# Kernel optimization log

Hardware: AMD Instinct MI355X
Metric: run time of the kernel (lower is better)

## Reference

```python
import jax, jax.numpy as jnp
import numpy as np

GAMMA = 0.9          # EMA momentum for prototype update
N_CLASSES = 201      # 200 classes + 1 background
K_PROTO = 5          # prototypes per class
FG_THRESH = 0.5      # pca_fg_threshold
SK_EPS = 0.05        # sinkhorn temperature (SwAV-style)
SK_ITERS = 3         # sinkhorn iterations
PCA_ITERS = 10       # niter of torch.pca_lowrank


def _l2norm(x, axis=-1):
    return x / jnp.maximum(jnp.linalg.norm(x, axis=axis, keepdims=True), 1e-12)


def _pca_first_component(X, key):
    # Randomized power iteration for the top left singular vector of the
    # centered data (mirrors torch.pca_lowrank(X, q=1, center=True, niter=10)).
    Xc = X - X.mean(0, keepdims=True)            # [N, D]
    G = Xc.T @ Xc                                # [D, D]
    v = jax.random.normal(key, (X.shape[1],), X.dtype)
    v = v / jnp.linalg.norm(v)
    def body(v, _):
        v = G @ v
        return v / jnp.maximum(jnp.linalg.norm(v), 1e-12), None
    v, _ = jax.lax.scan(body, v, None, length=PCA_ITERS)
    u = Xc @ v                                   # [N]
    return u / jnp.maximum(jnp.linalg.norm(u), 1e-12)


def _masked_sinkhorn(logits, mask):
    # logits: [C, BN, K], mask: [C, BN] bool (rows belonging to class c).
    # Vectorized equivalent of the per-class sinkhorn_knopp(L_c): returns a
    # row-stochastic assignment on the masked rows, balanced over the K cols.
    tiny = 1e-9
    m = mask[..., None].astype(logits.dtype)     # [C, BN, 1]
    Q = jnp.exp(logits / SK_EPS) * m
    n_c = jnp.maximum(mask.sum(-1).astype(logits.dtype), 1.0)[:, None, None]
    K = Q.shape[-1]
    Q = Q / jnp.maximum(Q.sum((-2, -1), keepdims=True), tiny)
    for _ in range(SK_ITERS):
        Q = Q / jnp.maximum(Q.sum(-2, keepdims=True), tiny) / K   # balance cols
        Q = Q * m
        Q = Q / jnp.maximum(Q.sum(-1, keepdims=True), tiny) / n_c # balance rows
        Q = Q * m
    return Q * n_c  # each masked row sums to 1


def setup_inputs() -> dict:
    key = jax.random.key(0)
    k1, k2, k3 = jax.random.split(key, 3)
    B, n_patches, dim = 32, 1024, 768
    patch_tokens = jax.random.normal(k1, (B, n_patches, dim), jnp.float32)
    prototypes = 0.02 * jax.random.normal(k2, (N_CLASSES, K_PROTO, dim), jnp.float32)
    labels = jax.random.randint(k3, (B,), 0, 200).astype(jnp.int64)
    return {"patch_tokens": patch_tokens, "prototypes": prototypes, "labels": labels}


def reference(patch_tokens, prototypes, labels):
    B, n_patches, D = patch_tokens.shape

    pt_norm = _l2norm(patch_tokens)              # [B, N, D]
    proto_norm = _l2norm(prototypes)             # [C, K, D]
    # B n_patches dim, C K dim -> B n_patches C K
    logits = jnp.einsum('bnd,ckd->bnck', pt_norm, proto_norm)

    # ---- get_pseudo_patch_labels (PCA foreground extraction) ----
    X = patch_tokens.reshape(-1, D)
    U = _pca_first_component(X, jax.random.key(1))
    U_scaled = (U - U.min()) / (U.max() - U.min())
    fg = (U_scaled < FG_THRESH).reshape(B, n_patches)
    patch_labels = jnp.where(fg, labels[:, None], N_CLASSES - 1)  # [B, N] int

    # ---- update_prototypes, vectorized over the 201-class python loop ----
    pl_flat = patch_labels.reshape(-1)                            # [B*N]
    L = jnp.transpose(logits.reshape(-1, N_CLASSES, K_PROTO), (1, 0, 2))  # [C, BN, K]
    class_ids = jnp.arange(N_CLASSES)
    mask = pl_flat[None, :] == class_ids[:, None]                 # [C, BN]
    Q = _masked_sinkhorn(L, mask)                                 # [C, BN, K]
    # P_c_new = L_c_assignment.T @ I_c, batched over classes
    P_new = jnp.einsum('cnk,nd->ckd', Q, pt_norm.reshape(-1, D))  # [C, K, D]
    present = (labels[None, :] == class_ids[:, None]).any(-1)     # 'c in labels'
    ema = GAMMA * prototypes + (1.0 - GAMMA) * P_new              # momentum_update
    new_prototypes = jnp.where(present[:, None, None], ema, prototypes)

    image_prototype_logits = logits.max(1)        # [B, C, K]
    class_logits = image_prototype_logits.sum(-1) # [B, C]
    return class_logits, image_prototype_logits, new_prototypes
```

## Files before the change

kernel.cpp:

```cpp
#include <hip/hip_runtime.h>
#include <stdint.h>
#include <stddef.h>

#define DEV static __device__ __forceinline__

typedef __attribute__((ext_vector_type(8))) short bf16x8;
typedef __attribute__((ext_vector_type(4))) float f32x4;
typedef __attribute__((ext_vector_type(4))) int i32x4;

DEV float bf2f(unsigned short u){ union{unsigned int i; float f;} v; v.i = ((unsigned int)u)<<16; return v.f; }
DEV unsigned short f2bf(float f){ union{float f; unsigned int i;} v; v.f=f; unsigned int i=v.i;
  return (unsigned short)((i + 0x7FFFu + ((i>>16)&1u)) >> 16); }
DEV unsigned int fenc(float x){ unsigned int i = __float_as_uint(x); return (i & 0x80000000u) ? ~i : (i | 0x80000000u); }
DEV float fdec(unsigned int e){ unsigned int i = (e & 0x80000000u) ? (e & 0x7FFFFFFFu) : ~e; return __uint_as_float(i); }

DEV float waveSum(float s){
  for (int m=32;m;m>>=1) s += __shfl_xor(s, m, 64);
  return s;
}

DEV float blockSum(float v, float* red){
  int t = threadIdx.x;
  red[t] = v; __syncthreads();
  for (int k=128;k>0;k>>=1){ if (t<k) red[t] += red[t+k]; __syncthreads(); }
  float r = red[0]; __syncthreads();
  return r;
}

DEV void gl16(const void* g, void* lds){
  __builtin_amdgcn_global_load_lds(
      (const __attribute__((address_space(1))) void*)g,
      (__attribute__((address_space(3))) void*)lds, 16, 0, 0);
}

DEV float erfinv_f(float x){
  float w = -log1pf(-__fmul_rn(x,x));
  float p;
  if (w < 5.0f){
    w = w - 2.5f;
    p = 2.81022636e-08f;
    p = 3.43273939e-07f + p*w;
    p = -3.5233877e-06f + p*w;
    p = -4.39150654e-06f + p*w;
    p = 0.00021858087f + p*w;
    p = -0.00125372503f + p*w;
    p = -0.00417768164f + p*w;
    p = 0.246640727f + p*w;
    p = 1.50140941f + p*w;
  } else {
    w = sqrtf(w) - 3.0f;
    p = -0.000200214257f;
    p = 0.000100950558f + p*w;
    p = 0.00134934322f + p*w;
    p = -0.00367342844f + p*w;
    p = 0.00573950773f + p*w;
    p = -0.0076224613f + p*w;
    p = 0.00943887047f + p*w;
    p = 1.00167406f + p*w;
    p = 2.83297682f + p*w;
  }
  return p*x;
}

#define BN_TOT 32768
#define DIM 768
#define NCLS 201
#define KP 5
#define CKPAD 1024
#define NSPLIT_G 16
#define GSPLIT 32
#define PSPLIT 8
#define NBLK_G 672


__global__ void k_setup(unsigned int* ipl_enc, int* cnt, int* cur, int* present,
                        unsigned int* minmax, float* meansum,
                        const int* __restrict__ raw, int* __restrict__ lab,
                        float* __restrict__ v,
                        const float* __restrict__ protos, unsigned short* __restrict__ protn,
                        int* __restrict__ dcnt){
  int i = blockIdx.x*256 + threadIdx.x;
  ipl_enc[i] = 0u;
  if (i < NCLS){ cnt[i]=0; cur[i]=0; present[i]=0; }
  if (i < DIM) meansum[i] = 0.f;
  if (i == 0){
    minmax[0]=0xFFFFFFFFu; minmax[1]=0u;
    dcnt[0] = 0;
    bool is64 = true;
    for (int j=0;j<8;j++){
      int lo = raw[2*j], hi = raw[2*j+1];
      if (hi != 0 || lo < 0 || lo >= NCLS-1){ is64 = false; break; }
    }
    for (int j=0;j<32;j++) lab[j] = is64 ? raw[2*j] : raw[j];
  }
  if (i < DIM){
    unsigned int ks[3] = {0u, 1u, 0x1BD11BDBu};
    const int rot0[4] = {13,15,26,6};
    const int rot1[4] = {17,29,16,24};
    unsigned int x0 = 0u, x1 = (unsigned int)i;
    x0 += ks[0]; x1 += ks[1];
    #pragma unroll
    for (int g=0; g<5; g++){
      const int* rr = (g&1) ? rot1 : rot0;
      #pragma unroll
      for (int j=0;j<4;j++){
        x0 += x1;
        x1 = (x1 << rr[j]) | (x1 >> (32-rr[j]));
        x1 ^= x0;
      }
      x0 += ks[(g+1)%3];
      x1 += ks[(g+2)%3] + (unsigned int)(g+1);
    }
    unsigned int b = x0 ^ x1;
    const float lo = __uint_as_float(0xBF7FFFFFu);
    const float sq2 = __uint_as_float(0x3FB504F3u);
    float f = __uint_as_float((b>>9) | 0x3F800000u) - 1.0f;
    float uu = __fadd_rn(__fmul_rn(f, 2.0f), lo);
    uu = fmaxf(lo, uu);
    v[i] = sq2 * erfinv_f(uu);
  }
  int l = threadIdx.x & 63;
  #pragma unroll
  for (int rr=0; rr<2; rr++){
    int row = blockIdx.x*8 + (threadIdx.x>>6)*2 + rr;
    if (row >= NCLS*KP){
      for (int j=0;j<12;j++) protn[(size_t)row*DIM + l + j*64] = 0;
    } else {
      const float* p = protos + (size_t)row*DIM;
      float x[12]; float s = 0.f;
      for (int j=0;j<12;j++){ x[j] = p[l + j*64]; s += x[j]*x[j]; }
      s = waveSum(s);
      float inv = 1.0f / fmaxf(sqrtf(s), 1e-12f);
      for (int j=0;j<12;j++) protn[(size_t)row*DIM + l + j*64] = f2bf(x[j]*inv);
    }
  }
}

__global__ void k_trans(const float* __restrict__ X, signed char* __restrict__ q1T,
                        signed char* __restrict__ q2T, float* __restrict__ meansum){
  __shared__ float tile[64][65];
  __shared__ float colsum[4][64];
  int n0 = blockIdx.x*64, c0 = blockIdx.y*64;
  int t = threadIdx.x;
  float part = 0.f;
  for (int i=0;i<16;i++){
    int idx = t + i*256; int r = idx>>6, c = idx&63;
    float x = X[(size_t)(n0+r)*DIM + c0+c];
    tile[r][c] = x;
    part += x;
  }
  colsum[t>>6][t&63] = part;
  __syncthreads();
  for (int i=0;i<4;i++){
    int flat = t + i*256;
    int c = flat>>4;
    int ng = flat&15;
    unsigned int p1 = 0, p2 = 0;
    #pragma unroll
    for (int j=0;j<4;j++){
      float x = tile[ng*4+j][c];
      int q1 = (int)rintf(x*16.0f);
      q1 = max(-127, min(127, q1));
      float r2 = x - (float)q1*(1.0f/16.0f);
      int q2 = (int)rintf(r2*2048.0f);
      q2 = max(-127, min(127, q2));
      p1 |= ((unsigned int)(q1 & 0xff)) << (8*j);
      p2 |= ((unsigned int)(q2 & 0xff)) << (8*j);
    }
    size_t o = (size_t)(c0+c)*BN_TOT + n0 + ng*4;
    *(unsigned int*)&q1T[o] = p1;
    *(unsigned int*)&q2T[o] = p2;
  }
  if (t < 64){
    float s = colsum[0][t]+colsum[1][t]+colsum[2][t]+colsum[3][t];
    atomicAdd(&meansum[c0+t], s);
  }
}

__global__ void k_ptn(const float* __restrict__ X, unsigned short* __restrict__ ptn){
  int row = blockIdx.x*4 + (threadIdx.x>>6);
  int l = threadIdx.x & 63;
  const float4* xr = (const float4*)(X + (size_t)row*DIM);
  float4 x4[3]; float s = 0.f;
  #pragma unroll
  for (int j=0;j<3;j++){
    x4[j] = xr[l + j*64];
    s += x4[j].x*x4[j].x + x4[j].y*x4[j].y + x4[j].z*x4[j].z + x4[j].w*x4[j].w;
  }
  s = waveSum(s);
  float inv = 1.0f / fmaxf(sqrtf(s), 1e-12f);
  #pragma unroll
  for (int j=0;j<3;j++){
    ushort4 o;
    o.x = f2bf(x4[j].x*inv); o.y = f2bf(x4[j].y*inv);
    o.z = f2bf(x4[j].z*inv); o.w = f2bf(x4[j].w*inv);
    *(ushort4*)&ptn[(size_t)row*DIM + 4*(l + j*64)] = o;
  }
}

DEV void g_coords(int b, int& s, int& ib, int& jb){
  int xcd = b & 7, q = b >> 3;
  s = xcd + 8*(q/21);
  int p = q % 21;
  ib = 0; int rem = p;
  while (rem >= 6 - ib){ rem -= 6 - ib; ib++; }
  jb = ib + rem;
}

__global__ __launch_bounds__(256) void k_mega(const signed char* __restrict__ q1T,
                                              const signed char* __restrict__ q2T,
                                              float* __restrict__ Gpart,
                                              const unsigned short* __restrict__ A,
                                              const unsigned short* __restrict__ Bt,
                                              unsigned int* __restrict__ ipl_enc){
  __shared__ __align__(16) signed char LB[32768];
  __shared__ float red[2][2][64];
  int bid = blockIdx.x;
  int t = threadIdx.x, w = t>>6, l = t&63;
  int wr = w>>1, wc = w&1;

  if (bid < NBLK_G){
    int chain2 = (bid >= 21*NSPLIT_G);
    int s, ib, jb; g_coords(chain2 ? bid - 21*NSPLIT_G : bid, s, ib, jb);
    size_t baseA = (size_t)(ib*128)*BN_TOT;
    size_t baseB = (size_t)(jb*128)*BN_TOT;

    i32x4 acc[4][4];
    #pragma unroll
    for (int m=0;m<4;m++)
      #pragma unroll
      for (int n=0;n<4;n++){ acc[m][n][0]=0; acc[m][n][1]=0; acc[m][n][2]=0; acc[m][n][3]=0; }

    float scale;
    if (!chain2){
      signed char* A1 = LB;
      signed char* B1 = LB + 16384;
      int gu = (l&7) ^ ((l>>3)&7);
      size_t lane_off = (size_t)(l>>3)*BN_TOT + (size_t)gu*16;
      for (int kt=0; kt<16; kt++){
        size_t k0 = (size_t)s*2048 + (size_t)kt*128;
        __syncthreads();
        #pragma unroll
        for (int ci=0; ci<4; ci++){
          int rg = w + ci*4;
          size_t roff = (size_t)(rg*8)*BN_TOT + k0 + lane_off;
          gl16(q1T + baseA + roff, A1 + rg*1024);
          gl16(q1T + baseB + roff, B1 + rg*1024);
        }
        __syncthreads();
        #pragma unroll
        for (int kk=0; kk<2; kk++){
          int physb = (((kk*4) + (l>>4)) ^ (l&7))*16;
          i32x4 b1[4];
          #pragma unroll
          for (int n=0;n<4;n++) b1[n] = *(const i32x4*)&B1[(wc*64 + n*16 + (l&15))*128 + physb];
          #pragma unroll
          for (int m=0;m<4;m++){
            i32x4 a1 = *(const i32x4*)&A1[(wr*64 + m*16 + (l&15))*128 + physb];
            #pragma unroll
            for (int n=0;n<4;n++)
              acc[m][n] = __builtin_amdgcn_mfma_i32_16x16x64_i8(a1, b1[n], acc[m][n], 0,0,0);
          }
        }
      }
      scale = 1.0f/256.0f;
    } else {
      signed char* A1 = LB;
      signed char* A2 = LB + 8192;
      signed char* B1 = LB + 16384;
      signed char* B2 = LB + 24576;
      int gu = (l&3) ^ ((l>>2)&3) ^ (l>>4);
      size_t lane_off = (size_t)(l>>2)*BN_TOT + (size_t)gu*16;
      int physc = (l>>4) ^ (l&3) ^ ((l>>2)&3);
      int rdA = (wr*64 + (l&15))*64 + physc*16;
      int rdB = (wc*64 + (l&15))*64 + physc*16;
      for (int kt=0; kt<32; kt++){
        size_t k0 = (size_t)s*2048 + (size_t)kt*64;
        __syncthreads();
        #pragma unroll
        for (int ci=0; ci<2; ci++){
          int c = w + ci*4;
          size_t roff = (size_t)(c*16)*BN_TOT + k0 + lane_off;
          gl16(q1T + baseA + roff, A1 + c*1024);
          gl16(q2T + baseA + roff, A2 + c*1024);
          gl16(q1T + baseB + roff, B1 + c*1024);
          gl16(q2T + baseB + roff, B2 + c*1024);
        }
        __syncthreads();
        i32x4 b1[4], b2[4];
        #pragma unroll
        for (int n=0;n<4;n++){
          b1[n] = *(const i32x4*)&B1[rdB + n*1024];
          b2[n] = *(const i32x4*)&B2[rdB + n*1024];
        }
        #pragma unroll
        for (int m=0;m<4;m++){
          i32x4 a1 = *(const i32x4*)&A1[rdA + m*1024];
          i32x4 a2 = *(const i32x4*)&A2[rdA + m*1024];
          #pragma unroll
          for (int n=0;n<4;n++){
            acc[m][n] = __builtin_amdgcn_mfma_i32_16x16x64_i8(a1, b2[n], acc[m][n], 0,0,0);
            acc[m][n] = __builtin_amdgcn_mfma_i32_16x16x64_i8(a2, b1[n], acc[m][n], 0,0,0);
          }
        }
      }
      scale = 1.0f/32768.0f;
    }

    int slice = chain2 ? (NSPLIT_G + s) : s;
    float* out = Gpart + (size_t)slice*DIM*DIM;
    #pragma unroll
    for (int m=0;m<4;m++)
      #pragma unroll
      for (int n=0;n<4;n++)
        #pragma unroll
        for (int r=0;r<4;r++){
          int row = ib*128 + wr*64 + m*16 + (l>>4)*4 + r;
          int col = jb*128 + wc*64 + n*16 + (l&15);
          float val = (float)acc[m][n][r]*scale;
          out[(size_t)row*DIM + col] = val;
          if (ib != jb) out[(size_t)col*DIM + row] = val;
        }
  } else {
    unsigned short* As = (unsigned short*)LB;
    unsigned short* Bs = (unsigned short*)(LB + 16384);
    int flat = bid - NBLK_G;
    int xcd = flat & 7, j = flat >> 3;
    int mb = xcd*32 + (j>>3);
    int nb = j & 7;

    int gu = (l&7) ^ ((l>>3)&7);
    size_t lane_off = (size_t)(l>>3)*DIM + (size_t)gu*8;
    size_t baseA = (size_t)(mb*128)*DIM;
    size_t baseB = (size_t)(nb*128)*DIM;

    f32x4 acc[4][4];
    #pragma unroll
    for (int m=0;m<4;m++)
      #pragma unroll
      for (int n=0;n<4;n++){ acc[m][n][0]=0.f; acc[m][n][1]=0.f; acc[m][n][2]=0.f; acc[m][n][3]=0.f; }

    for (int kt=0; kt<12; kt++){
      size_t k0 = (size_t)kt*64;
      __syncthreads();
      #pragma unroll
      for (int ci=0; ci<4; ci++){
        int rg = w + ci*4;
        size_t roff = (size_t)(rg*8)*DIM + k0 + lane_off;
        gl16(A + baseA + roff, &As[rg*512]);
        gl16(Bt + baseB + roff, &Bs[rg*512]);
      }
      __syncthreads();
      #pragma unroll
      for (int kk=0; kk<2; kk++){
        int physb = (((kk*4) + (l>>4)) ^ (l&7))*8;
        bf16x8 a[4], b[4];
        #pragma unroll
        for (int m=0;m<4;m++) a[m] = *(const bf16x8*)&As[(wr*64 + m*16 + (l&15))*64 + physb];
        #pragma unroll
        for (int n=0;n<4;n++) b[n] = *(const bf16x8*)&Bs[(wc*64 + n*16 + (l&15))*64 + physb];
        #pragma unroll
        for (int m=0;m<4;m++)
          #pragma unroll
          for (int n=0;n<4;n++)
            acc[m][n] = __builtin_amdgcn_mfma_f32_16x16x32_bf16(a[m], b[n], acc[m][n], 0,0,0);
      }
    }
    float vmax[4];
    #pragma unroll
    for (int n=0;n<4;n++){
      float v = -1e30f;
      #pragma unroll
      for (int m=0;m<4;m++)
        #pragma unroll
        for (int r=0;r<4;r++) v = fmaxf(v, acc[m][n][r]);
      v = fmaxf(v, __shfl_xor(v, 16, 64));
      v = fmaxf(v, __shfl_xor(v, 32, 64));
      vmax[n] = v;
    }
    __syncthreads();
    if (l < 16){
      #pragma unroll
      for (int n=0;n<4;n++) red[wc][wr][n*16 + l] = vmax[n];
    }
    __syncthreads();
    if (t < 128){
      int wcc = t>>6, col = t&63;
      float v = fmaxf(red[wcc][0][col], red[wcc][1][col]);
      int gcol = nb*128 + wcc*64 + col;
      if (gcol < NCLS*KP){
        int b = (mb*128) >> 10;
        atomicMax(&ipl_enc[b*CKPAD + gcol], fenc(v));
      }
    }
  }
}

__global__ void k_gfix(const float* __restrict__ Gpart, const float* __restrict__ meansum,
                       float* __restrict__ G){
  int i4 = blockIdx.x*256 + threadIdx.x;
  int i = i4*4;
  int r = i/DIM, c = i%DIM;
  float4 s = make_float4(0.f,0.f,0.f,0.f);
  for (int p=0;p<GSPLIT;p++){
    float4 g = *(const float4*)&Gpart[(size_t)p*DIM*DIM + i];
    s.x += g.x; s.y += g.y; s.z += g.z; s.w += g.w;
  }
  const float invN = 1.0f/32768.0f;
  float mr = meansum[r]*invN;
  float4 mc = *(const float4*)&meansum[c];
  float4 o;
  o.x = s.x*invN - mr*mc.x*invN;
  o.y = s.y*invN - mr*mc.y*invN;
  o.z = s.z*invN - mr*mc.z*invN;
  o.w = s.w*invN - mr*mc.w*invN;
  *(float4*)&G[i] = o;
}

__global__ void k_mv(const float* __restrict__ G, const float* __restrict__ vin,
                     float* __restrict__ vout){
  __shared__ float vs[DIM];
  int t = threadIdx.x;
  for (int i=t;i<DIM;i+=256) vs[i] = vin[i];
  __syncthreads();
  int row = blockIdx.x*4 + (t>>6), l = t&63;
  const float* g = G + (size_t)row*DIM;
  float s = 0.f;
  for (int j=0;j<12;j++) s += g[l + j*64]*vs[l + j*64];
  s = waveSum(s);
  if (l==0) vout[row] = s;
}

__global__ void k_u(const float* __restrict__ X, const float* __restrict__ v,
                    const float* __restrict__ meansum,
                    float* __restrict__ u, unsigned int* __restrict__ minmax){
  __shared__ float vs[DIM];
  __shared__ float red[256];
  __shared__ float smn[4], smx[4];
  int t = threadIdx.x;
  for (int i=t;i<DIM;i+=256) vs[i] = v[i];
  __syncthreads();
  float ps = 0.f;
  for (int i=t;i<DIM;i+=256) ps += meansum[i]*(1.0f/32768.0f)*vs[i];
  float scal = blockSum(ps, red);
  int w = t>>6, l = t&63;
  float mn = 1e30f, mx = -1e30f;
  #pragma unroll
  for (int rr=0; rr<4; rr++){
    int row = blockIdx.x*16 + w*4 + rr;
    const float4* xr = (const float4*)(X + (size_t)row*DIM);
    float s = 0.f;
    #pragma unroll
    for (int j=0;j<3;j++){
      float4 x4 = xr[l + j*64];
      int base = 4*(l + j*64);
      s += x4.x*vs[base] + x4.y*vs[base+1] + x4.z*vs[base+2] + x4.w*vs[base+3];
    }
    s = waveSum(s);
    if (l==0){
      float val = s - scal;
      u[row] = val;
      mn = fminf(mn, val); mx = fmaxf(mx, val);
    }
  }
  if (l==0){ smn[w]=mn; smx[w]=mx; }
  __syncthreads();
  if (t==0){
    for (int k=1;k<4;k++){ mn = fminf(mn, smn[k]); mx = fmaxf(mx, smx[k]); }
    atomicMin(&minmax[0], fenc(mn));
    atomicMax(&minmax[1], fenc(mx));
  }
}

__global__ void k_pl(const float* __restrict__ u, const int* __restrict__ labels,
                     const unsigned int* __restrict__ minmax, int* __restrict__ pl,
                     int* __restrict__ cnt, int* __restrict__ offs,
                     int* __restrict__ present, int* __restrict__ dcnt){
  int n = blockIdx.x*256 + threadIdx.x;
  int t = threadIdx.x;
  float umin = fdec(minmax[0]), umax = fdec(minmax[1]);
  float us = (u[n]-umin)/(umax-umin);
  int c = (us < 0.5f) ? labels[n>>10] : (NCLS-1);
  pl[n] = c;
  if (c < NCLS-1) atomicAdd(&cnt[c], 1);
  __threadfence();
  __shared__ int lastblk;
  if (t == 0) lastblk = (atomicAdd(dcnt, 1) == 127) ? 1 : 0;
  __syncthreads();
  if (lastblk){
    __shared__ int sc[256];
    sc[t] = (t < NCLS-1) ? atomicAdd(&cnt[t], 0) : 0;
    __syncthreads();
    for (int d=1; d<256; d<<=1){
      int v = (t >= d) ? sc[t-d] : 0;
      __syncthreads();
      sc[t] += v;
      __syncthreads();
    }
    if (t < NCLS) offs[t] = (t == 0) ? 0 : sc[t-1];
    if (t < 32) atomicOr(&present[labels[t]], 1);
  }
}

__global__ void k_scatter(const int* __restrict__ pl, const int* __restrict__ offs,
                          int* __restrict__ cur, int* __restrict__ idx){
  int n = blockIdx.x*256 + threadIdx.x;
  int c = pl[n];
  if (c < NCLS-1){
    int p = offs[c] + atomicAdd(&cur[c], 1);
    idx[p] = n;
  }
}

__global__ void k_qlog(const int* __restrict__ idx, const int* __restrict__ offs,
                       const int* __restrict__ pl, const unsigned short* __restrict__ ptn,
                       const unsigned short* __restrict__ protn, float* __restrict__ q){
  int i = blockIdx.x*4 + (threadIdx.x>>6);
  int l = threadIdx.x & 63;
  int total = offs[NCLS-1];
  if (i >= total) return;
  int n = idx[i];
  int c = pl[n];
  const unsigned short* pr = ptn + (size_t)n*DIM;
  float x[12];
  for (int j=0;j<12;j++) x[j] = bf2f(pr[l + j*64]);
  for (int k=0;k<KP;k++){
    const unsigned short* wv = protn + (size_t)(c*KP + k)*DIM;
    float s = 0.f;
    for (int j=0;j<12;j++) s += x[j]*bf2f(wv[l + j*64]);
    s = waveSum(s);
    if (l==0) q[(size_t)i*KP + k] = expf(s*20.0f);
  }
}

__global__ void k_sink(const int* __restrict__ cnt, const int* __restrict__ offs,
                       float* __restrict__ q){
  __shared__ float red[256];
  __shared__ float colf[KP];
  int c = blockIdx.x;
  int nc = cnt[c];
  if (nc == 0) return;
  int n0 = offs[c];
  float* Q = q + (size_t)n0*KP;
  int t = threadIdx.x;
  int tot5 = nc*KP;
  float s = 0.f;
  for (int i=t;i<tot5;i+=256) s += Q[i];
  float total = blockSum(s, red);
  float sc = 1.0f/fmaxf(total, 1e-9f);
  for (int i=t;i<tot5;i+=256) Q[i] *= sc;
  __syncthreads();
  float ncf = (float)nc;
  for (int it=0; it<3; it++){
    float cs[KP] = {0,0,0,0,0};
    for (int i=t;i<nc;i+=256){
      const float* row = Q + (size_t)i*KP;
      #pragma unroll
      for (int k=0;k<KP;k++) cs[k] += row[k];
    }
    for (int k=0;k<KP;k++){
      float v = blockSum(cs[k], red);
      if (t==0) colf[k] = 1.0f/(fmaxf(v,1e-9f)*(float)KP);
    }
    __syncthreads();
    for (int i=t;i<nc;i+=256){
      float* row = Q + (size_t)i*KP;
      float qq[KP]; float rs = 0.f;
      #pragma unroll
      for (int k=0;k<KP;k++){ qq[k] = row[k]*colf[k]; rs += qq[k]; }
      float rf = 1.0f/(fmaxf(rs,1e-9f)*ncf);
      #pragma unroll
      for (int k=0;k<KP;k++) row[k] = qq[k]*rf;
    }
    __syncthreads();
  }
  for (int i=t;i<tot5;i+=256) Q[i] *= ncf;
}

__global__ void k_pnew(const int* __restrict__ cnt, const int* __restrict__ offs,
                       const int* __restrict__ present, const int* __restrict__ idx,
                       const float* __restrict__ q, const unsigned short* __restrict__ ptn,
                       float* __restrict__ P4){
  int c = blockIdx.y, s = blockIdx.x;
  if (!present[c]) return;
  int nc = cnt[c], n0 = offs[c];
  int r0 = n0 + (nc*s)/PSPLIT;
  int r1 = n0 + (nc*(s+1))/PSPLIT;
  int t = threadIdx.x;
  float acc[KP][3];
  #pragma unroll
  for (int k=0;k<KP;k++){ acc[k][0]=0.f; acc[k][1]=0.f; acc[k][2]=0.f; }
  for (int i=r0; i<r1; ++i){
    int n = idx[i];
    float qv[KP];
    #pragma unroll
    for (int k=0;k<KP;k++) qv[k] = q[(size_t)i*KP + k];
    const unsigned short* row = ptn + (size_t)n*DIM;
    #pragma unroll
    for (int j=0;j<3;j++){
      float x = bf2f(row[t + j*256]);
      #pragma unroll
      for (int k=0;k<KP;k++) acc[k][j] += qv[k]*x;
    }
  }
  float* out = P4 + ((size_t)(s*NCLS + c)*KP)*DIM;
  #pragma unroll
  for (int k=0;k<KP;k++)
    #pragma unroll
    for (int j=0;j<3;j++)
      out[(size_t)k*DIM + t + j*256] = acc[k][j];
}

__global__ void k_emafinal(const float* __restrict__ protos, const float* __restrict__ P4,
                           const int* __restrict__ present,
                           const unsigned int* __restrict__ ipl_enc,
                           float* __restrict__ out){
  int bid = blockIdx.x;
  if (bid < 3015){
    int i = bid*256 + threadIdx.x;
    if (i >= NCLS*KP*DIM) return;
    int c = i / (KP*DIM);
    float p = protos[i];
    float* o = out + 32*NCLS + 32*NCLS*KP;
    if (present[c]){
      float s = 0.f;
      #pragma unroll
      for (int sp=0; sp<PSPLIT; sp++) s += P4[(size_t)sp*NCLS*KP*DIM + i];
      o[i] = 0.9f*p + 0.1f*s;
    } else {
      o[i] = p;
    }
  } else {
    int i = (bid-3015)*256 + threadIdx.x;
    if (i < 32*NCLS*KP){
      int b = i / (NCLS*KP), ck = i % (NCLS*KP);
      out[32*NCLS + i] = fdec(ipl_enc[b*CKPAD + ck]);
    }
    if (i < 32*NCLS){
      int b = i / NCLS, c = i % NCLS;
      float s = 0.f;
      #pragma unroll
      for (int k=0;k<KP;k++) s += fdec(ipl_enc[b*CKPAD + c*KP + k]);
      out[b*NCLS + c] = s;
    }
  }
}

extern "C" void kernel_launch(void* const* d_in, const int* in_sizes, int n_in,
                              void* d_out, int out_size, void* d_ws, size_t ws_size,
                              hipStream_t stream){
  (void)in_sizes; (void)n_in; (void)out_size; (void)ws_size;
  const float* X = (const float*)d_in[0];
  const float* protos = (const float*)d_in[1];
  const int* labels_raw = (const int*)d_in[2];
  float* out = (float*)d_out;

  char* w = (char*)d_ws;
  size_t off = 0;
  auto alloc = [&](size_t bytes)->void*{
    void* p = (void*)(w + off);
    off = (off + bytes + 255) & ~(size_t)255;
    return p;
  };
  signed char* q1T      = (signed char*)alloc((size_t)DIM*BN_TOT);
  signed char* q2T      = (signed char*)alloc((size_t)DIM*BN_TOT);
  unsigned short* ptn   = (unsigned short*)alloc((size_t)BN_TOT*DIM*2);
  unsigned short* protn = (unsigned short*)alloc((size_t)CKPAD*DIM*2);
  float* Gpart   = (float*)alloc((size_t)GSPLIT*DIM*DIM*4);
  float* G       = (float*)alloc((size_t)DIM*DIM*4);
  float* meansum = (float*)alloc(DIM*4);
  float* vA      = (float*)alloc(DIM*4);
  float* vB      = (float*)alloc(DIM*4);
  int* cnt       = (int*)alloc(1024);
  int* cur       = (int*)alloc(1024);
  int* offs      = (int*)alloc(1024);
  int* present   = (int*)alloc(1024);
  int* labc      = (int*)alloc(256);
  int* dcnt      = (int*)alloc(256);
  unsigned int* minmax  = (unsigned int*)alloc(256);
  unsigned int* ipl_enc = (unsigned int*)alloc((size_t)32*CKPAD*4);

  char* gb = (char*)Gpart;
  size_t goff = 0;
  auto galloc = [&](size_t bytes)->void*{
    void* p = (void*)(gb + goff);
    goff = (goff + bytes + 255) & ~(size_t)255;
    return p;
  };
  float* u_  = (float*)galloc(BN_TOT*4);
  int* pl_   = (int*)galloc(BN_TOT*4);
  int* idx_  = (int*)galloc(BN_TOT*4);
  float* q_  = (float*)galloc((size_t)BN_TOT*KP*4);
  float* P4_ = (float*)galloc((size_t)PSPLIT*NCLS*KP*DIM*4);

  dim3 b256(256);
  k_setup<<<dim3(128), b256, 0, stream>>>(ipl_enc, cnt, cur, present, minmax, meansum,
                                          labels_raw, labc, vA, protos, protn, dcnt);
  k_trans<<<dim3(512,12), b256, 0, stream>>>(X, q1T, q2T, meansum);
  k_ptn<<<dim3(8192), b256, 0, stream>>>(X, ptn);
  k_mega<<<dim3(NBLK_G + 2048), b256, 0, stream>>>(q1T, q2T, Gpart, ptn, protn, ipl_enc);
  k_gfix<<<dim3(576), b256, 0, stream>>>(Gpart, meansum, G);
  for (int it=0; it<10; it++){
    float* src = (it&1) ? vB : vA;
    float* dst = (it&1) ? vA : vB;
    k_mv<<<dim3(192), b256, 0, stream>>>(G, src, dst);
  }
  k_u<<<dim3(2048), b256, 0, stream>>>(X, vA, meansum, u_, minmax);
  k_pl<<<dim3(128), b256, 0, stream>>>(u_, labc, minmax, pl_, cnt, offs, present, dcnt);
  k_scatter<<<dim3(128), b256, 0, stream>>>(pl_, offs, cur, idx_);
  k_qlog<<<dim3(8192), b256, 0, stream>>>(idx_, offs, pl_, ptn, protn, q_);
  k_sink<<<dim3(200), b256, 0, stream>>>(cnt, offs, q_);
  k_pnew<<<dim3(PSPLIT,NCLS), b256, 0, stream>>>(cnt, offs, present, idx_, q_, ptn, P4_);
  k_emafinal<<<dim3(3141), b256, 0, stream>>>(protos, P4_, present, ipl_enc, out);
}
```

Before: 443.4 us.

## Fuse transpose/quantize with normalize pass and fold P_new into sinkhorn kernel

Merges k_trans and k_ptn into a single k_prep kernel. Each block loads 16 rows of X into shared memory once and produces both the bf16 normalized rows and the transposed int8 split quantization, so X is read from global memory once instead of twice. It also moves the P_new accumulation into k_sink, which removes k_pnew and the 8-way partial buffer. The cost is that each class's accumulation is serialized in one block instead of split 8 ways, which may lengthen the tail for large classes such as background. The k_prep stores are 16-byte column writes into a strided transposed layout.

```diff
diff --git a/kernel.cpp b/kernel.cpp
--- a/kernel.cpp
+++ b/kernel.cpp
@@ -69,7 +69,6 @@
 #define CKPAD 1024
 #define NSPLIT_G 16
 #define GSPLIT 32
-#define PSPLIT 8
 #define NBLK_G 672
 
 
@@ -136,65 +135,72 @@
   }
 }
 
-__global__ void k_trans(const float* __restrict__ X, signed char* __restrict__ q1T,
-                        signed char* __restrict__ q2T, float* __restrict__ meansum){
-  __shared__ float tile[64][65];
-  __shared__ float colsum[4][64];
-  int n0 = blockIdx.x*64, c0 = blockIdx.y*64;
+__global__ __launch_bounds__(256) void k_prep(const float* __restrict__ X,
+                                              unsigned short* __restrict__ ptn,
+                                              signed char* __restrict__ q1T,
+                                              signed char* __restrict__ q2T,
+                                              float* __restrict__ meansum){
+  __shared__ float tile[16][DIM];
+  int bid = blockIdx.x;
+  int xcd = bid & 7, j = bid >> 3;
+  int n0 = xcd*4096 + j*16;
   int t = threadIdx.x;
-  float part = 0.f;
-  for (int i=0;i<16;i++){
-    int idx = t + i*256; int r = idx>>6, c = idx&63;
-    float x = X[(size_t)(n0+r)*DIM + c0+c];
-    tile[r][c] = x;
-    part += x;
-  }
-  colsum[t>>6][t&63] = part;
+  {
+    const float4* src = (const float4*)(X + (size_t)n0*DIM);
+    float4* dst = (float4*)&tile[0][0];
+    #pragma unroll
+    for (int i=0;i<12;i++) dst[t + i*256] = src[t + i*256];
+  }
   __syncthreads();
-  for (int i=0;i<4;i++){
-    int flat = t + i*256;
-    int c = flat>>4;
-    int ng = flat&15;
-    unsigned int p1 = 0, p2 = 0;
-    #pragma unroll
-    for (int j=0;j<4;j++){
-      float x = tile[ng*4+j][c];
-      int q1 = (int)rintf(x*16.0f);
-      q1 = max(-127, min(127, q1));
-      float r2 = x - (float)q1*(1.0f/16.0f);
-      int q2 = (int)rintf(r2*2048.0f);
-      q2 = max(-127, min(127, q2));
-      p1 |= ((unsigned int)(q1 & 0xff)) << (8*j);
-      p2 |= ((unsigned int)(q2 & 0xff)) << (8*j);
-    }
-    size_t o = (size_t)(c0+c)*BN_TOT + n0 + ng*4;
-    *(unsigned int*)&q1T[o] = p1;
-    *(unsigned int*)&q2T[o] = p2;
-  }
-  if (t < 64){
-    float s = colsum[0][t]+colsum[1][t]+colsum[2][t]+colsum[3][t];
-    atomicAdd(&meansum[c0+t], s);
-  }
-}
-
-__global__ void k_ptn(const float* __restrict__ X, unsigned short* __restrict__ ptn){
-  int row = blockIdx.x*4 + (threadIdx.x>>6);
-  int l = threadIdx.x & 63;
-  const float4* xr = (const float4*)(X + (size_t)row*DIM);
-  float4 x4[3]; float s = 0.f;
+  int w = t>>6, l = t&63;
   #pragma unroll
-  for (int j=0;j<3;j++){
-    x4[j] = xr[l + j*64];
-    s += x4[j].x*x4[j].x + x4[j].y*x4[j].y + x4[j].z*x4[j].z + x4[j].w*x4[j].w;
-  }
-  s = waveSum(s);
-  float inv = 1.0f / fmaxf(sqrtf(s), 1e-12f);
+  for (int rr=0; rr<4; rr++){
+    int r = w*4 + rr;
+    const float4* xr = (const float4*)&tile[r][0];
+    float4 x4[3]; float s = 0.f;
+    #pragma unroll
+    for (int jj=0;jj<3;jj++){
+      x4[jj] = xr[l + jj*64];
+      s += x4[jj].x*x4[jj].x + x4[jj].y*x4[jj].y + x4[jj].z*x4[jj].z + x4[jj].w*x4[jj].w;
+    }
+    s = waveSum(s);
+    float inv = 1.0f / fmaxf(sqrtf(s), 1e-12f);
+    #pragma unroll
+    for (int jj=0;jj<3;jj++){
+      ushort4 o;
+      o.x = f2bf(x4[jj].x*inv); o.y = f2bf(x4[jj].y*inv);
+      o.z = f2bf(x4[jj].z*inv); o.w = f2bf(x4[jj].w*inv);
+      *(ushort4*)&ptn[(size_t)(n0+r)*DIM + 4*(l + jj*64)] = o;
+    }
+  }
   #pragma unroll
-  for (int j=0;j<3;j++){
-    ushort4 o;
-    o.x = f2bf(x4[j].x*inv); o.y = f2bf(x4[j].y*inv);
-    o.z = f2bf(x4[j].z*inv); o.w = f2bf(x4[j].w*inv);
-    *(ushort4*)&ptn[(size_t)row*DIM + 4*(l + j*64)] = o;
+  for (int cc=0; cc<3; cc++){
+    int c = t + cc*256;
+    unsigned int u1[4], u2[4];
+    #pragma unroll
+    for (int g=0; g<4; g++){
+      unsigned int p1 = 0, p2 = 0;
+      #pragma unroll
+      for (int k=0;k<4;k++){
+        float xx = tile[g*4+k][c];
+        int v1 = (int)rintf(xx*16.0f);
+        v1 = max(-127, min(127, v1));
+        float r2 = xx - (float)v1*(1.0f/16.0f);
+        int v2 = (int)rintf(r2*2048.0f);
+        v2 = max(-127, min(127, v2));
+        p1 |= ((unsigned int)(v1 & 0xff)) << (8*k);
+        p2 |= ((unsigned int)(v2 & 0xff)) << (8*k);
+      }
+      u1[g] = p1; u2[g] = p2;
+    }
+    uint4 a; a.x=u1[0]; a.y=u1[1]; a.z=u1[2]; a.w=u1[3];
+    uint4 b; b.x=u2[0]; b.y=u2[1]; b.z=u2[2]; b.w=u2[3];
+    *(uint4*)&q1T[(size_t)c*BN_TOT + n0] = a;
+    *(uint4*)&q2T[(size_t)c*BN_TOT + n0] = b;
+    float s = 0.f;
+    #pragma unroll
+    for (int r=0;r<16;r++) s += tile[r][c];
+    atomicAdd(&meansum[c], s);
   }
 }
 
@@ -534,15 +540,27 @@
 }
 
 __global__ void k_sink(const int* __restrict__ cnt, const int* __restrict__ offs,
-                       float* __restrict__ q){
+                       float* __restrict__ q, const int* __restrict__ present,
+                       const int* __restrict__ idx, const unsigned short* __restrict__ ptn,
+                       float* __restrict__ P){
   __shared__ float red[256];
   __shared__ float colf[KP];
   int c = blockIdx.x;
   int nc = cnt[c];
-  if (nc == 0) return;
+  int t = threadIdx.x;
+  if (nc == 0){
+    if (present[c]){
+      float* Pout = P + (size_t)c*KP*DIM;
+      #pragma unroll
+      for (int k=0;k<KP;k++)
+        #pragma unroll
+        for (int jj=0;jj<3;jj++)
+          Pout[(size_t)k*DIM + t + jj*256] = 0.f;
+    }
+    return;
+  }
   int n0 = offs[c];
   float* Q = q + (size_t)n0*KP;
-  int t = threadIdx.x;
   int tot5 = nc*KP;
   float s = 0.f;
   for (int i=t;i<tot5;i+=256) s += Q[i];
@@ -575,43 +593,32 @@
     __syncthreads();
   }
   for (int i=t;i<tot5;i+=256) Q[i] *= ncf;
-}
-
-__global__ void k_pnew(const int* __restrict__ cnt, const int* __restrict__ offs,
-                       const int* __restrict__ present, const int* __restrict__ idx,
-                       const float* __restrict__ q, const unsigned short* __restrict__ ptn,
-                       float* __restrict__ P4){
-  int c = blockIdx.y, s = blockIdx.x;
   if (!present[c]) return;
-  int nc = cnt[c], n0 = offs[c];
-  int r0 = n0 + (nc*s)/PSPLIT;
-  int r1 = n0 + (nc*(s+1))/PSPLIT;
-  int t = threadIdx.x;
+  __syncthreads();
   float acc[KP][3];
   #pragma unroll
   for (int k=0;k<KP;k++){ acc[k][0]=0.f; acc[k][1]=0.f; acc[k][2]=0.f; }
-  for (int i=r0; i<r1; ++i){
-    int n = idx[i];
+  for (int i=0;i<nc;i++){
+    int n = idx[n0 + i];
     float qv[KP];
     #pragma unroll
-    for (int k=0;k<KP;k++) qv[k] = q[(size_t)i*KP + k];
-    const unsigned short* row = ptn + (size_t)n*DIM;
-    #pragma unroll
-    for (int j=0;j<3;j++){
-      float x = bf2f(row[t + j*256]);
-      #pragma unroll
-      for (int k=0;k<KP;k++) acc[k][j] += qv[k]*x;
-    }
-  }
-  float* out = P4 + ((size_t)(s*NCLS + c)*KP)*DIM;
+    for (int k=0;k<KP;k++) qv[k] = Q[(size_t)i*KP + k];
+    #pragma unroll
+    for (int jj=0;jj<3;jj++){
+      float x = bf2f(ptn[(size_t)n*DIM + t + jj*256]);
+      #pragma unroll
+      for (int k=0;k<KP;k++) acc[k][jj] += qv[k]*x;
+    }
+  }
+  float* Pout = P + (size_t)c*KP*DIM;
   #pragma unroll
   for (int k=0;k<KP;k++)
     #pragma unroll
-    for (int j=0;j<3;j++)
-      out[(size_t)k*DIM + t + j*256] = acc[k][j];
-}
-
-__global__ void k_emafinal(const float* __restrict__ protos, const float* __restrict__ P4,
+    for (int jj=0;jj<3;jj++)
+      Pout[(size_t)k*DIM + t + jj*256] = acc[k][jj];
+}
+
+__global__ void k_emafinal(const float* __restrict__ protos, const float* __restrict__ P,
                            const int* __restrict__ present,
                            const unsigned int* __restrict__ ipl_enc,
                            float* __restrict__ out){
@@ -622,14 +629,7 @@
     int c = i / (KP*DIM);
     float p = protos[i];
     float* o = out + 32*NCLS + 32*NCLS*KP;
-    if (present[c]){
-      float s = 0.f;
-      #pragma unroll
-      for (int sp=0; sp<PSPLIT; sp++) s += P4[(size_t)sp*NCLS*KP*DIM + i];
-      o[i] = 0.9f*p + 0.1f*s;
-    } else {
-      o[i] = p;
-    }
+    o[i] = present[c] ? (0.9f*p + 0.1f*P[i]) : p;
   } else {
     int i = (bid-3015)*256 + threadIdx.x;
     if (i < 32*NCLS*KP){
@@ -691,13 +691,12 @@
   int* pl_   = (int*)galloc(BN_TOT*4);
   int* idx_  = (int*)galloc(BN_TOT*4);
   float* q_  = (float*)galloc((size_t)BN_TOT*KP*4);
-  float* P4_ = (float*)galloc((size_t)PSPLIT*NCLS*KP*DIM*4);
+  float* P_  = (float*)galloc((size_t)NCLS*KP*DIM*4);
 
   dim3 b256(256);
   k_setup<<<dim3(128), b256, 0, stream>>>(ipl_enc, cnt, cur, present, minmax, meansum,
                                           labels_raw, labc, vA, protos, protn, dcnt);
-  k_trans<<<dim3(512,12), b256, 0, stream>>>(X, q1T, q2T, meansum);
-  k_ptn<<<dim3(8192), b256, 0, stream>>>(X, ptn);
+  k_prep<<<dim3(2048), b256, 0, stream>>>(X, ptn, q1T, q2T, meansum);
   k_mega<<<dim3(NBLK_G + 2048), b256, 0, stream>>>(q1T, q2T, Gpart, ptn, protn, ipl_enc);
   k_gfix<<<dim3(576), b256, 0, stream>>>(Gpart, meansum, G);
   for (int it=0; it<10; it++){
@@ -709,7 +708,6 @@
   k_pl<<<dim3(128), b256, 0, stream>>>(u_, labc, minmax, pl_, cnt, offs, present, dcnt);
   k_scatter<<<dim3(128), b256, 0, stream>>>(pl_, offs, cur, idx_);
   k_qlog<<<dim3(8192), b256, 0, stream>>>(idx_, offs, pl_, ptn, protn, q_);
-  k_sink<<<dim3(200), b256, 0, stream>>>(cnt, offs, q_);
-  k_pnew<<<dim3(PSPLIT,NCLS), b256, 0, stream>>>(cnt, offs, present, idx_, q_, ptn, P4_);
-  k_emafinal<<<dim3(3141), b256, 0, stream>>>(protos, P4_, present, ipl_enc, out);
-}
+  k_sink<<<dim3(200), b256, 0, stream>>>(cnt, offs, q_, present, idx_, ptn, P_);
+  k_emafinal<<<dim3(3141), b256, 0, stream>>>(protos, P_, present, ipl_enc, out);
+}
```

After: 681.2 us. 53.6% more time.
